# Kernel optimization log

Hardware: AMD Instinct MI355X
Metric: run time of the kernel (lower is better)

Reference implementation:

```python
import jax, jax.numpy as jnp
import numpy as np

N = 8192      # neurons per layer (and n_inputs)
L = 16        # hidden topological layers
DEG = 128     # avg in-degree
E = N * DEG   # edges per hidden layer
NOUT = 16     # output neurons
EOUT = N * NOUT  # edges into output layer


def _lrelu(v):
    return jnp.where(v >= 0, v, 0.01 * v)


def setup_inputs() -> dict:
    key = jax.random.key(0)
    ks = jax.random.split(key, 7)
    x = jax.random.normal(ks[0], (N,), dtype=jnp.float32)
    edge_src = jax.random.randint(ks[1], (L, E), 0, N, dtype=jnp.int32)
    edge_dst = jax.random.randint(ks[2], (L, E), 0, N, dtype=jnp.int32)
    # scale weights ~1/sqrt(degree) so 16 layers of accumulation stay finite
    edge_w = jax.random.normal(ks[3], (L, E), dtype=jnp.float32) / np.float32(np.sqrt(DEG))
    out_src = jax.random.randint(ks[4], (EOUT,), 0, N, dtype=jnp.int32)
    out_dst = jax.random.randint(ks[5], (EOUT,), 0, NOUT, dtype=jnp.int32)
    out_w = jax.random.normal(ks[6], (EOUT,), dtype=jnp.float32) / np.float32(np.sqrt(EOUT / NOUT))
    return {"x": x, "edge_w": edge_w, "out_w": out_w,
            "edge_src": edge_src, "edge_dst": edge_dst,
            "out_src": out_src, "out_dst": out_dst}


def reference(x, edge_w, out_w, edge_src, edge_dst, out_src, out_dst):
    n = x.shape[0]

    def step(vals, layer):
        src, dst, w = layer
        # per-node weighted accumulation: n.value += i.value * i.weight[n]
        new = jax.ops.segment_sum(vals[src] * w, dst, num_segments=n)
        return _lrelu(new), None  # leaky_relu on every non-INPUT node

    vals, _ = jax.lax.scan(step, x, (edge_src, edge_dst, edge_w))
    o = jax.ops.segment_sum(vals[out_src] * out_w, out_dst, num_segments=NOUT)
    o = _lrelu(o)
    return jax.nn.softmax(o, axis=0)
```

## Files before the change

kernel.cpp:

```cpp
#include <hip/hip_runtime.h>

#define NN    8192
#define NL    16
#define NE    (NN * 128)
#define NOUTC 16
#define EOUTC (NN * NOUTC)

#define NBLK  256
#define NTHR  512
#define EPB   (NE / NBLK)

__device__ __forceinline__ float lrelu(float v) { return v >= 0.f ? v : 0.01f * v; }

__global__ __launch_bounds__(256) void zero_kernel(float* __restrict__ p, int n) {
    int i = blockIdx.x * 256 + threadIdx.x;
    if (i < n) p[i] = 0.f;
}

__global__ __launch_bounds__(NTHR) void layer_kernel(
    const float* __restrict__ sv,
    const int    apply_act,
    const int*   __restrict__ es,
    const int*   __restrict__ ed,
    const float* __restrict__ ew,
    float*       __restrict__ accL)
{
    __shared__ float vals[NN];
    __shared__ float accs[NN];
    const int tid = threadIdx.x;
    const int b   = blockIdx.x;

    for (int i = tid * 4; i < NN; i += NTHR * 4) {
        float4 v = *(const float4*)(sv + i);
        if (apply_act) {
            v.x = lrelu(v.x); v.y = lrelu(v.y);
            v.z = lrelu(v.z); v.w = lrelu(v.w);
        }
        *(float4*)(vals + i) = v;
        *(float4*)(accs + i) = make_float4(0.f, 0.f, 0.f, 0.f);
    }
    __syncthreads();

    const int base = b * EPB;
    #pragma unroll
    for (int it = 0; it < EPB / (NTHR * 4); ++it) {
        const int e = base + it * NTHR * 4 + tid * 4;
        int4   s = *(const int4*)(es + e);
        int4   d = *(const int4*)(ed + e);
        float4 w = *(const float4*)(ew + e);
        atomicAdd(&accs[d.x], vals[s.x] * w.x);
        atomicAdd(&accs[d.y], vals[s.y] * w.y);
        atomicAdd(&accs[d.z], vals[s.z] * w.z);
        atomicAdd(&accs[d.w], vals[s.w] * w.w);
    }
    __syncthreads();

    for (int i = tid; i < NN; i += NTHR) {
        float v = accs[i];
        if (v != 0.f) atomicAdd(accL + i, v);
    }
}

__global__ __launch_bounds__(NTHR) void out_kernel(
    const float* __restrict__ acc15,
    const int*   __restrict__ out_src,
    const int*   __restrict__ out_dst,
    const float* __restrict__ out_w,
    float*       __restrict__ outacc)
{
    __shared__ float bins[NOUTC];
    const int tid = threadIdx.x;
    if (tid < NOUTC) bins[tid] = 0.f;
    __syncthreads();
    const int g = blockIdx.x * NTHR + tid;
    const float v = lrelu(acc15[out_src[g]]);
    atomicAdd(&bins[out_dst[g]], v * out_w[g]);
    __syncthreads();
    if (tid < NOUTC) atomicAdd(&outacc[tid], bins[tid]);
}

__global__ __launch_bounds__(64) void softmax_kernel(
    const float* __restrict__ outacc, float* __restrict__ out)
{
    const int lane = threadIdx.x;
    float v = (lane < NOUTC) ? lrelu(outacc[lane]) : -INFINITY;
    float m = v;
    #pragma unroll
    for (int off = 32; off >= 1; off >>= 1)
        m = fmaxf(m, __shfl_xor(m, off, 64));
    float e = (lane < NOUTC) ? __expf(v - m) : 0.f;
    float s = e;
    #pragma unroll
    for (int off = 32; off >= 1; off >>= 1)
        s += __shfl_xor(s, off, 64);
    if (lane < NOUTC) out[lane] = e / s;
}

extern "C" void kernel_launch(void* const* d_in, const int* in_sizes, int n_in,
                              void* d_out, int out_size, void* d_ws, size_t ws_size,
                              hipStream_t stream) {
    const float* x        = (const float*)d_in[0];
    const float* edge_w   = (const float*)d_in[1];
    const float* out_w    = (const float*)d_in[2];
    const int*   edge_src = (const int*)d_in[3];
    const int*   edge_dst = (const int*)d_in[4];
    const int*   out_src  = (const int*)d_in[5];
    const int*   out_dst  = (const int*)d_in[6];

    float* acc    = (float*)d_ws;
    float* outacc = acc + (size_t)NL * NN;
    float* out    = (float*)d_out;

    const int nz = NL * NN + NOUTC;
    zero_kernel<<<(nz + 255) / 256, 256, 0, stream>>>(acc, nz);

    for (int l = 0; l < NL; ++l) {
        const float* sv = (l == 0) ? x : (acc + (size_t)(l - 1) * NN);
        layer_kernel<<<NBLK, NTHR, 0, stream>>>(
            sv, l > 0,
            edge_src + (size_t)l * NE,
            edge_dst + (size_t)l * NE,
            edge_w   + (size_t)l * NE,
            acc + (size_t)l * NN);
    }

    out_kernel<<<NBLK, NTHR, 0, stream>>>(
        acc + (size_t)(NL - 1) * NN, out_src, out_dst, out_w, outacc);

    softmax_kernel<<<1, 64, 0, stream>>>(outacc, out);
}
```

Measured before the change: 434.5 us.

## Replace global atomic accumulation with per-block partials and a separate reduction kernel

Each scatter block now writes its full shared-memory accumulator to a private row of a partials buffer instead of issuing global atomics. A new reduce kernel sums the 256 rows per neuron, applies leaky ReLU, and writes the activation vector that the next layer reads. The output stage follows the same pattern: per-block bins are reduced in a final kernel that also does the softmax. This removes the zero-init kernel and the global atomic contention. In exchange it adds 16 extra launches and writes and reads about 8 MB of partials per layer.

```diff
diff --git a/kernel.cpp b/kernel.cpp
--- a/kernel.cpp
+++ b/kernel.cpp
@@ -12,18 +12,12 @@
 
 __device__ __forceinline__ float lrelu(float v) { return v >= 0.f ? v : 0.01f * v; }
 
-__global__ __launch_bounds__(256) void zero_kernel(float* __restrict__ p, int n) {
-    int i = blockIdx.x * 256 + threadIdx.x;
-    if (i < n) p[i] = 0.f;
-}
-
-__global__ __launch_bounds__(NTHR) void layer_kernel(
+__global__ __launch_bounds__(NTHR) void scatter_kernel(
     const float* __restrict__ sv,
-    const int    apply_act,
     const int*   __restrict__ es,
     const int*   __restrict__ ed,
     const float* __restrict__ ew,
-    float*       __restrict__ accL)
+    float*       __restrict__ partials)
 {
     __shared__ float vals[NN];
     __shared__ float accs[NN];
@@ -31,12 +25,7 @@
     const int b   = blockIdx.x;
 
     for (int i = tid * 4; i < NN; i += NTHR * 4) {
-        float4 v = *(const float4*)(sv + i);
-        if (apply_act) {
-            v.x = lrelu(v.x); v.y = lrelu(v.y);
-            v.z = lrelu(v.z); v.w = lrelu(v.w);
-        }
-        *(float4*)(vals + i) = v;
+        *(float4*)(vals + i) = *(const float4*)(sv + i);
         *(float4*)(accs + i) = make_float4(0.f, 0.f, 0.f, 0.f);
     }
     __syncthreads();
@@ -55,45 +44,80 @@
     }
     __syncthreads();
 
-    for (int i = tid; i < NN; i += NTHR) {
-        float v = accs[i];
-        if (v != 0.f) atomicAdd(accL + i, v);
+    float* prow = partials + (size_t)b * NN;
+    for (int i = tid * 4; i < NN; i += NTHR * 4)
+        *(float4*)(prow + i) = *(const float4*)(accs + i);
+}
+
+__global__ __launch_bounds__(256) void reduce_kernel(
+    const float* __restrict__ partials,
+    float*       __restrict__ accv)
+{
+    __shared__ float sred[8][32];
+    const int b  = blockIdx.x;
+    const int nl = threadIdx.x & 31;
+    const int kg = threadIdx.x >> 5;
+    const int n  = b * 32 + nl;
+
+    float s = 0.f;
+    #pragma unroll
+    for (int k = 0; k < NBLK / 8; ++k)
+        s += partials[(size_t)(kg + k * 8) * NN + n];
+    sred[kg][nl] = s;
+    __syncthreads();
+    if (threadIdx.x < 32) {
+        float t = 0.f;
+        #pragma unroll
+        for (int j = 0; j < 8; ++j) t += sred[j][threadIdx.x];
+        accv[b * 32 + threadIdx.x] = lrelu(t);
     }
 }
 
-__global__ __launch_bounds__(NTHR) void out_kernel(
-    const float* __restrict__ acc15,
+__global__ __launch_bounds__(NTHR) void out_scatter_kernel(
+    const float* __restrict__ accv,
     const int*   __restrict__ out_src,
     const int*   __restrict__ out_dst,
     const float* __restrict__ out_w,
-    float*       __restrict__ outacc)
+    float*       __restrict__ outs)
 {
     __shared__ float bins[NOUTC];
     const int tid = threadIdx.x;
     if (tid < NOUTC) bins[tid] = 0.f;
     __syncthreads();
     const int g = blockIdx.x * NTHR + tid;
-    const float v = lrelu(acc15[out_src[g]]);
-    atomicAdd(&bins[out_dst[g]], v * out_w[g]);
+    atomicAdd(&bins[out_dst[g]], accv[out_src[g]] * out_w[g]);
     __syncthreads();
-    if (tid < NOUTC) atomicAdd(&outacc[tid], bins[tid]);
+    if (tid < NOUTC) outs[(size_t)blockIdx.x * NOUTC + tid] = bins[tid];
 }
 
-__global__ __launch_bounds__(64) void softmax_kernel(
-    const float* __restrict__ outacc, float* __restrict__ out)
+__global__ __launch_bounds__(256) void final_kernel(
+    const float* __restrict__ outs, float* __restrict__ out)
 {
-    const int lane = threadIdx.x;
-    float v = (lane < NOUTC) ? lrelu(outacc[lane]) : -INFINITY;
-    float m = v;
+    __shared__ float red[16][17];
+    const int tid = threadIdx.x;
+    const int j = tid & 15, g = tid >> 4;
+    float s = 0.f;
     #pragma unroll
-    for (int off = 32; off >= 1; off >>= 1)
-        m = fmaxf(m, __shfl_xor(m, off, 64));
-    float e = (lane < NOUTC) ? __expf(v - m) : 0.f;
-    float s = e;
-    #pragma unroll
-    for (int off = 32; off >= 1; off >>= 1)
-        s += __shfl_xor(s, off, 64);
-    if (lane < NOUTC) out[lane] = e / s;
+    for (int r = 0; r < NBLK / 16; ++r)
+        s += outs[(size_t)(g + r * 16) * NOUTC + j];
+    red[g][j] = s;
+    __syncthreads();
+    if (tid < NOUTC) {
+        float t = 0.f;
+        #pragma unroll
+        for (int g2 = 0; g2 < 16; ++g2) t += red[g2][tid];
+        float v = lrelu(t);
+        float m = v;
+        #pragma unroll
+        for (int off = 8; off >= 1; off >>= 1)
+            m = fmaxf(m, __shfl_xor(m, off, 64));
+        float e = __expf(v - m);
+        float ssum = e;
+        #pragma unroll
+        for (int off = 8; off >= 1; off >>= 1)
+            ssum += __shfl_xor(ssum, off, 64);
+        out[tid] = e / ssum;
+    }
 }
 
 extern "C" void kernel_launch(void* const* d_in, const int* in_sizes, int n_in,
@@ -107,25 +131,22 @@
     const int*   out_src  = (const int*)d_in[5];
     const int*   out_dst  = (const int*)d_in[6];
 
-    float* acc    = (float*)d_ws;
-    float* outacc = acc + (size_t)NL * NN;
-    float* out    = (float*)d_out;
-
-    const int nz = NL * NN + NOUTC;
-    zero_kernel<<<(nz + 255) / 256, 256, 0, stream>>>(acc, nz);
+    float* partials = (float*)d_ws;
+    float* accv     = partials + (size_t)NBLK * NN;
+    float* outs     = accv + NN;
+    float* out      = (float*)d_out;
 
     for (int l = 0; l < NL; ++l) {
-        const float* sv = (l == 0) ? x : (acc + (size_t)(l - 1) * NN);
-        layer_kernel<<<NBLK, NTHR, 0, stream>>>(
-            sv, l > 0,
+        const float* sv = (l == 0) ? x : accv;
+        scatter_kernel<<<NBLK, NTHR, 0, stream>>>(
+            sv,
             edge_src + (size_t)l * NE,
             edge_dst + (size_t)l * NE,
             edge_w   + (size_t)l * NE,
-            acc + (size_t)l * NN);
+            partials);
+        reduce_kernel<<<NBLK, 256, 0, stream>>>(partials, accv);
     }
 
-    out_kernel<<<NBLK, NTHR, 0, stream>>>(
-        acc + (size_t)(NL - 1) * NN, out_src, out_dst, out_w, outacc);
-
-    softmax_kernel<<<1, 64, 0, stream>>>(outacc, out);
+    out_scatter_kernel<<<NBLK, NTHR, 0, stream>>>(accv, out_src, out_dst, out_w, outs);
+    final_kernel<<<1, 256, 0, stream>>>(outs, out);
 }
```

New measurement: 401.6 us. 1.08x faster.
